# Optimization experiments

Measured on AMD Instinct MI355X. Metric: run time of the kernel, lower is better.

Reference implementation:

```python
import jax, jax.numpy as jnp
import numpy as np

N_ELEC = 1536
SPINS = (768, 768)
L = 20.0
HID = 16


def _block_masks(spins, n):
    # blkdiag_mask: same-spin pairs (block diagonal); offdiag_mask: opposite-spin pairs
    cum = np.cumsum([0, *spins])
    off = np.ones((n, n), dtype=bool)
    for i, j in zip(cum[:-1], cum[1:]):
        off[i:j, i:j] = False
    return jnp.asarray(~off), jnp.asarray(off)


def _eta_mlp(s, W1, b1, W2, b2, W3, b3):
    # per-pair scalar MLP: (n,n) -> (n,n)
    h = jnp.tanh(s[..., None] * W1[0] + b1)      # (n,n,HID)
    h = jnp.tanh(h @ W2 + b2)                    # (n,n,HID)
    return (h @ W3 + b3)[..., 0]                 # (n,n)


def setup_inputs() -> dict:
    key = jax.random.key(0)
    ks = jax.random.split(key, 8)
    inp = {
        "x": jax.random.uniform(ks[0], (N_ELEC, 3), jnp.float32) * L,
        "cell": L * jnp.eye(3, dtype=jnp.float32),
        "Wp1": jax.random.normal(ks[1], (1, HID), jnp.float32),
        "bp1": jnp.zeros((HID,), jnp.float32),
        "Wp2": jax.random.normal(ks[2], (HID, HID), jnp.float32) / np.sqrt(HID),
        "bp2": jnp.zeros((HID,), jnp.float32),
        "Wp3": jax.random.normal(ks[3], (HID, 1), jnp.float32) / np.sqrt(HID),
        "bp3": jnp.zeros((1,), jnp.float32),
        "Wa1": jax.random.normal(ks[4], (1, HID), jnp.float32),
        "ba1": jnp.zeros((HID,), jnp.float32),
        "Wa2": jax.random.normal(ks[5], (HID, HID), jnp.float32) / np.sqrt(HID),
        "ba2": jnp.zeros((HID,), jnp.float32),
        "Wa3": jax.random.normal(ks[6], (HID, 1), jnp.float32) / np.sqrt(HID),
        "ba3": jnp.zeros((1,), jnp.float32),
        "n_up": SPINS[0],
    }
    return inp


def reference(x, cell, Wp1, bp1, Wp2, bp2, Wp3, bp3,
              Wa1, ba1, Wa2, ba2, Wa3, ba3, n_up):
    n = x.shape[-2]
    ndim = 3
    spins = (int(n_up), n - int(n_up))
    blkdiag_mask, offdiag_mask = _block_masks(spins, n)

    # r_s of the homogeneous electron gas
    vol_pp = jnp.abs(jnp.linalg.det(cell)) / n
    rs = (2 * (ndim - 1) * jnp.pi / (ndim * vol_pp)) ** (-1.0 / ndim)

    # periodic (half-sinusoid) displacement features
    frac = x @ jnp.linalg.inv(cell)                      # (n,3)
    d_frac = frac[:, None, :] - frac[None, :, :]         # (n,n,3)
    d_hsin = jnp.sin(jnp.pi * d_frac) @ cell / jnp.pi    # (n,n,3)
    eye = jnp.eye(n, dtype=x.dtype)
    # safe norm: diagonal pairs are masked out of eta anyway
    dist = jnp.sqrt(jnp.sum(d_hsin * d_hsin, axis=-1) + eye)

    x_by_rs = dist / rs
    eta = _eta_mlp(x_by_rs, Wp1, bp1, Wp2, bp2, Wp3, bp3) * blkdiag_mask * (1 - eye)
    eta = eta + _eta_mlp(x_by_rs, Wa1, ba1, Wa2, ba2, Wa3, ba3) * offdiag_mask

    dr = jnp.einsum('ij,ijl->jl', eta, -d_hsin)          # (n,3)
    return x + dr
```

## Files before the change

### kernel.cpp

```cpp
#include <hip/hip_runtime.h>
#include <math.h>

#define HID   16
#define BLK   256
#define TBL_N 4096

__device__ __forceinline__ float fast_tanh(float x) {
    float ax = fabsf(x);
    float t  = __expf(-2.0f * ax);
    float r  = (1.0f - t) * __builtin_amdgcn_rcpf(1.0f + t);
    return copysignf(r, x);
}

__device__ __forceinline__ float eta_mlp(float s,
    const float* __restrict__ W1, const float* __restrict__ b1,
    const float* __restrict__ W2, const float* __restrict__ b2,
    const float* __restrict__ W3, const float* __restrict__ b3)
{
    float g[HID];
#pragma unroll
    for (int l = 0; l < HID; ++l) g[l] = fast_tanh(fmaf(s, W1[l], b1[l]));
    float t[HID];
#pragma unroll
    for (int l = 0; l < HID; ++l) t[l] = b2[l];
#pragma unroll
    for (int m = 0; m < HID; ++m) {
        float gm = g[m];
#pragma unroll
        for (int l = 0; l < HID; ++l) t[l] = fmaf(gm, W2[m * HID + l], t[l]);
    }
    float eta = b3[0];
#pragma unroll
    for (int l = 0; l < HID; ++l) eta = fmaf(fast_tanh(t[l]), W3[l], eta);
    return eta;
}

__device__ __forceinline__ void derive_consts(const float* __restrict__ cell,
                                              int n, float* inv_rs, float* smax_s)
{
    const float m00=cell[0],m01=cell[1],m02=cell[2];
    const float m10=cell[3],m11=cell[4],m12=cell[5];
    const float m20=cell[6],m21=cell[7],m22=cell[8];
    const float det = m00*(m11*m22-m12*m21)-m01*(m10*m22-m12*m20)+m02*(m10*m21-m11*m20);
    const float PI = 3.14159265358979323846f;
    const float vol_pp = fabsf(det) / (float)n;
    *inv_rs = cbrtf(4.0f * PI / (3.0f * vol_pp));
    const float r0 = sqrtf(m00*m00+m01*m01+m02*m02);
    const float r1 = sqrtf(m10*m10+m11*m11+m12*m12);
    const float r2 = sqrtf(m20*m20+m21*m21+m22*m22);
    *smax_s = (r0 + r1 + r2) * (1.0f / PI) * (*inv_rs) * 1.0005f;
}

extern "C" __global__ void build_tables(
    const float* __restrict__ x, const float* __restrict__ cell,
    const float* __restrict__ Wp1, const float* __restrict__ bp1,
    const float* __restrict__ Wp2, const float* __restrict__ bp2,
    const float* __restrict__ Wp3, const float* __restrict__ bp3,
    const float* __restrict__ Wa1, const float* __restrict__ ba1,
    const float* __restrict__ Wa2, const float* __restrict__ ba2,
    const float* __restrict__ Wa3, const float* __restrict__ ba3,
    float2* __restrict__ tbl, float4* __restrict__ frac, int n)
{
    const int t = blockIdx.x * blockDim.x + threadIdx.x;

    if (t < 2 * TBL_N) {
        const int bank = (t >= TBL_N) ? 1 : 0;
        const int idx  = bank ? (t - TBL_N) : t;

        float inv_rs, smax;
        derive_consts(cell, n, &inv_rs, &smax);
        const float ds = smax / (float)(TBL_N - 1);
        const float s  = idx * ds;

        float v0, v1;
        if (bank == 0) {
            v0 = eta_mlp(s,      Wp1, bp1, Wp2, bp2, Wp3, bp3);
            v1 = eta_mlp(s + ds, Wp1, bp1, Wp2, bp2, Wp3, bp3);
        } else {
            v0 = eta_mlp(s,      Wa1, ba1, Wa2, ba2, Wa3, ba3);
            v1 = eta_mlp(s + ds, Wa1, ba1, Wa2, ba2, Wa3, ba3);
        }
        tbl[t] = make_float2(v0, v1 - v0);
        return;
    }

    const int i = t - 2 * TBL_N;
    if (i < n) {
        const float m00=cell[0],m01=cell[1],m02=cell[2];
        const float m10=cell[3],m11=cell[4],m12=cell[5];
        const float m20=cell[6],m21=cell[7],m22=cell[8];
        const float det = m00*(m11*m22-m12*m21)-m01*(m10*m22-m12*m20)+m02*(m10*m21-m11*m20);
        const float id  = 1.0f / det;
        const float i00=(m11*m22-m12*m21)*id, i01=(m02*m21-m01*m22)*id, i02=(m01*m12-m02*m11)*id;
        const float i10=(m12*m20-m10*m22)*id, i11=(m00*m22-m02*m20)*id, i12=(m02*m10-m00*m12)*id;
        const float i20=(m10*m21-m11*m20)*id, i21=(m01*m20-m00*m21)*id, i22=(m00*m11-m01*m10)*id;
        float x0 = x[i*3+0], x1 = x[i*3+1], x2 = x[i*3+2];
        float4 f;
        f.x = x0*i00 + x1*i10 + x2*i20;
        f.y = x0*i01 + x1*i11 + x2*i21;
        f.z = x0*i02 + x1*i12 + x2*i22;
        f.w = 0.0f;
        frac[i] = f;
    }
}

extern "C" __global__ __launch_bounds__(BLK)
void pair_backflow_main(
    const float* __restrict__ x, const float* __restrict__ cell,
    const int* __restrict__ n_up_ptr,
    const float2* __restrict__ tbl, const float4* __restrict__ frac,
    float* __restrict__ out, int n)
{
    __shared__ float sred[BLK / 64][3];

    const int tid = threadIdx.x;
    const int j   = blockIdx.x;

    const float m00=cell[0],m01=cell[1],m02=cell[2];
    const float m10=cell[3],m11=cell[4],m12=cell[5];
    const float m20=cell[6],m21=cell[7],m22=cell[8];
    const float IPI = 0.31830988618379067154f;
    const float c00=m00*IPI, c01=m01*IPI, c02=m02*IPI;
    const float c10=m10*IPI, c11=m11*IPI, c12=m12*IPI;
    const float c20=m20*IPI, c21=m21*IPI, c22=m22*IPI;

    float inv_rs, smax;
    derive_consts(cell, n, &inv_rs, &smax);
    const float c_u  = inv_rs * (float)(TBL_N - 1) / smax;
    const float umax = (float)(TBL_N - 1);

    const int  n_up = *n_up_ptr;
    const bool j_up = (j < n_up);
    const float4 fj = frac[j];

    float acc0 = 0.0f, acc1 = 0.0f, acc2 = 0.0f;

    for (int i = tid; i < n; i += BLK) {
        float4 fi = frac[i];
        float s0 = __builtin_amdgcn_sinf(0.5f * (fi.x - fj.x));
        float s1 = __builtin_amdgcn_sinf(0.5f * (fi.y - fj.y));
        float s2 = __builtin_amdgcn_sinf(0.5f * (fi.z - fj.z));
        float h0 = fmaf(s0, c00, fmaf(s1, c10, s2 * c20));
        float h1 = fmaf(s0, c01, fmaf(s1, c11, s2 * c21));
        float h2 = fmaf(s0, c02, fmaf(s1, c12, s2 * c22));
        float dist = sqrtf(fmaf(h0, h0, fmaf(h1, h1, h2 * h2)));

        float u   = fminf(dist * c_u, umax);
        int   idx = (int)u;
        float fr  = u - (float)idx;

        const bool same = ((i < n_up) == j_up);
        float2 e = tbl[(same ? 0 : TBL_N) + idx];
        float eta = fmaf(fr, e.y, e.x);
        eta = (i == j) ? 0.0f : eta;

        acc0 = fmaf(-eta, h0, acc0);
        acc1 = fmaf(-eta, h1, acc1);
        acc2 = fmaf(-eta, h2, acc2);
    }

#pragma unroll
    for (int off = 32; off > 0; off >>= 1) {
        acc0 += __shfl_xor(acc0, off);
        acc1 += __shfl_xor(acc1, off);
        acc2 += __shfl_xor(acc2, off);
    }
    const int lane = tid & 63;
    const int wid  = tid >> 6;
    if (lane == 0) {
        sred[wid][0] = acc0; sred[wid][1] = acc1; sred[wid][2] = acc2;
    }
    __syncthreads();
    if (tid < 3) {
        float dr = 0.0f;
#pragma unroll
        for (int wv = 0; wv < BLK / 64; ++wv) dr += sred[wv][tid];
        out[j * 3 + tid] = x[j * 3 + tid] + dr;
    }
}

extern "C" void kernel_launch(void* const* d_in, const int* in_sizes, int n_in,
                              void* d_out, int out_size, void* d_ws, size_t ws_size,
                              hipStream_t stream) {
    const float* x    = (const float*)d_in[0];
    const float* cell = (const float*)d_in[1];
    const float* Wp1  = (const float*)d_in[2];
    const float* bp1  = (const float*)d_in[3];
    const float* Wp2  = (const float*)d_in[4];
    const float* bp2  = (const float*)d_in[5];
    const float* Wp3  = (const float*)d_in[6];
    const float* bp3  = (const float*)d_in[7];
    const float* Wa1  = (const float*)d_in[8];
    const float* ba1  = (const float*)d_in[9];
    const float* Wa2  = (const float*)d_in[10];
    const float* ba2  = (const float*)d_in[11];
    const float* Wa3  = (const float*)d_in[12];
    const float* ba3  = (const float*)d_in[13];
    const int*   nup  = (const int*)d_in[14];
    float* out = (float*)d_out;

    const int n = in_sizes[0] / 3;

    float2* tbl  = (float2*)d_ws;
    float4* frac = (float4*)((char*)d_ws + (size_t)(2 * TBL_N) * sizeof(float2));

    const int work = 2 * TBL_N + n;
    build_tables<<<dim3((work + BLK - 1) / BLK), dim3(BLK), 0, stream>>>(
        x, cell, Wp1, bp1, Wp2, bp2, Wp3, bp3,
        Wa1, ba1, Wa2, ba2, Wa3, ba3, tbl, frac, n);

    pair_backflow_main<<<dim3(n), dim3(BLK), 0, stream>>>(
        x, cell, nup, tbl, frac, out, n);
}
```

Measured before the change: 97.72 us.

## Fuse table build and pair pass into one cooperative kernel, two rows per block

Merges the table-building and pair-accumulation kernels into a single cooperative launch separated by a grid-wide sync. Precomputed cell constants go into a small header, and spin flags plus half-angle scaling are packed into frac. Each block processes two output rows so every frac load is reused. The table stores single values, halving MLP evaluations, but lookups need two loads, and the grid sync plus the cooperative occupancy constraint are added costs.

```diff
diff --git a/kernel.cpp b/kernel.cpp
--- a/kernel.cpp
+++ b/kernel.cpp
@@ -1,9 +1,12 @@
 #include <hip/hip_runtime.h>
+#include <hip/hip_cooperative_groups.h>
 #include <math.h>
 
 #define HID   16
 #define BLK   256
 #define TBL_N 4096
+
+namespace cg = cooperative_groups;
 
 __device__ __forceinline__ float fast_tanh(float x) {
     float ax = fabsf(x);
@@ -51,41 +54,36 @@
     *smax_s = (r0 + r1 + r2) * (1.0f / PI) * (*inv_rs) * 1.0005f;
 }
 
-extern "C" __global__ void build_tables(
-    const float* __restrict__ x, const float* __restrict__ cell,
+extern "C" __global__ __launch_bounds__(BLK, 4)
+void pair_backflow_fused(
+    const float* __restrict__ x,   const float* __restrict__ cell,
     const float* __restrict__ Wp1, const float* __restrict__ bp1,
     const float* __restrict__ Wp2, const float* __restrict__ bp2,
     const float* __restrict__ Wp3, const float* __restrict__ bp3,
     const float* __restrict__ Wa1, const float* __restrict__ ba1,
     const float* __restrict__ Wa2, const float* __restrict__ ba2,
     const float* __restrict__ Wa3, const float* __restrict__ ba3,
-    float2* __restrict__ tbl, float4* __restrict__ frac, int n)
+    const int* __restrict__ n_up_ptr,
+    float* __restrict__ tbl, float4* __restrict__ frac, float* __restrict__ hdr,
+    float* __restrict__ out, int n)
 {
-    const int t = blockIdx.x * blockDim.x + threadIdx.x;
-
-    if (t < 2 * TBL_N) {
-        const int bank = (t >= TBL_N) ? 1 : 0;
-        const int idx  = bank ? (t - TBL_N) : t;
-
+    cg::grid_group gg = cg::this_grid();
+    const int tid = threadIdx.x;
+    const int g   = blockIdx.x * BLK + tid;
+
+    if (g <= 2 * TBL_N + 1) {
         float inv_rs, smax;
         derive_consts(cell, n, &inv_rs, &smax);
-        const float ds = smax / (float)(TBL_N - 1);
-        const float s  = idx * ds;
-
-        float v0, v1;
-        if (bank == 0) {
-            v0 = eta_mlp(s,      Wp1, bp1, Wp2, bp2, Wp3, bp3);
-            v1 = eta_mlp(s + ds, Wp1, bp1, Wp2, bp2, Wp3, bp3);
-        } else {
-            v0 = eta_mlp(s,      Wa1, ba1, Wa2, ba2, Wa3, ba3);
-            v1 = eta_mlp(s + ds, Wa1, ba1, Wa2, ba2, Wa3, ba3);
-        }
-        tbl[t] = make_float2(v0, v1 - v0);
-        return;
-    }
-
-    const int i = t - 2 * TBL_N;
-    if (i < n) {
+        const float ds  = smax / (float)(TBL_N - 1);
+        const int bank  = (g >= TBL_N) ? 1 : 0;
+        const int gg2   = (g >= 2 * TBL_N) ? (g - TBL_N) : g;
+        const int idx   = gg2 - bank * TBL_N;
+        const float s   = idx * ds;
+        float v = bank ? eta_mlp(s, Wa1, ba1, Wa2, ba2, Wa3, ba3)
+                       : eta_mlp(s, Wp1, bp1, Wp2, bp2, Wp3, bp3);
+        tbl[g] = v;
+    } else if (g < 2 * TBL_N + 2 + n) {
+        const int i = g - (2 * TBL_N + 2);
         const float m00=cell[0],m01=cell[1],m02=cell[2];
         const float m10=cell[3],m11=cell[4],m12=cell[5];
         const float m20=cell[6],m21=cell[7],m22=cell[8];
@@ -94,88 +92,105 @@
         const float i00=(m11*m22-m12*m21)*id, i01=(m02*m21-m01*m22)*id, i02=(m01*m12-m02*m11)*id;
         const float i10=(m12*m20-m10*m22)*id, i11=(m00*m22-m02*m20)*id, i12=(m02*m10-m00*m12)*id;
         const float i20=(m10*m21-m11*m20)*id, i21=(m01*m20-m00*m21)*id, i22=(m00*m11-m01*m10)*id;
+        const int n_up = *n_up_ptr;
         float x0 = x[i*3+0], x1 = x[i*3+1], x2 = x[i*3+2];
         float4 f;
-        f.x = x0*i00 + x1*i10 + x2*i20;
-        f.y = x0*i01 + x1*i11 + x2*i21;
-        f.z = x0*i02 + x1*i12 + x2*i22;
-        f.w = 0.0f;
+        f.x = 0.5f * (x0*i00 + x1*i10 + x2*i20);
+        f.y = 0.5f * (x0*i01 + x1*i11 + x2*i21);
+        f.z = 0.5f * (x0*i02 + x1*i12 + x2*i22);
+        f.w = (i < n_up) ? 0.0f : 1.0f;
         frac[i] = f;
-    }
-}
-
-extern "C" __global__ __launch_bounds__(BLK)
-void pair_backflow_main(
-    const float* __restrict__ x, const float* __restrict__ cell,
-    const int* __restrict__ n_up_ptr,
-    const float2* __restrict__ tbl, const float4* __restrict__ frac,
-    float* __restrict__ out, int n)
-{
-    __shared__ float sred[BLK / 64][3];
-
-    const int tid = threadIdx.x;
-    const int j   = blockIdx.x;
-
-    const float m00=cell[0],m01=cell[1],m02=cell[2];
-    const float m10=cell[3],m11=cell[4],m12=cell[5];
-    const float m20=cell[6],m21=cell[7],m22=cell[8];
-    const float IPI = 0.31830988618379067154f;
-    const float c00=m00*IPI, c01=m01*IPI, c02=m02*IPI;
-    const float c10=m10*IPI, c11=m11*IPI, c12=m12*IPI;
-    const float c20=m20*IPI, c21=m21*IPI, c22=m22*IPI;
-
-    float inv_rs, smax;
-    derive_consts(cell, n, &inv_rs, &smax);
-    const float c_u  = inv_rs * (float)(TBL_N - 1) / smax;
+    } else if (g == 2 * TBL_N + 2 + n) {
+        float inv_rs, smax;
+        derive_consts(cell, n, &inv_rs, &smax);
+        const float IPI = 0.31830988618379067154f;
+        hdr[0] = inv_rs * (float)(TBL_N - 1) / smax;
+        hdr[1] = cell[0]*IPI; hdr[2] = cell[1]*IPI; hdr[3] = cell[2]*IPI;
+        hdr[4] = cell[3]*IPI; hdr[5] = cell[4]*IPI; hdr[6] = cell[5]*IPI;
+        hdr[7] = cell[6]*IPI; hdr[8] = cell[7]*IPI; hdr[9] = cell[8]*IPI;
+    }
+
+    gg.sync();
+
+    const float c_u  = hdr[0];
+    const float c00 = hdr[1], c01 = hdr[2], c02 = hdr[3];
+    const float c10 = hdr[4], c11 = hdr[5], c12 = hdr[6];
+    const float c20 = hdr[7], c21 = hdr[8], c22 = hdr[9];
     const float umax = (float)(TBL_N - 1);
 
-    const int  n_up = *n_up_ptr;
-    const bool j_up = (j < n_up);
-    const float4 fj = frac[j];
-
-    float acc0 = 0.0f, acc1 = 0.0f, acc2 = 0.0f;
+    const int j0 = blockIdx.x;
+    const int j1 = blockIdx.x + (int)gridDim.x;
+    const bool has1 = (j1 < n);
+    const float4 fj0 = frac[j0];
+    const float4 fj1 = has1 ? frac[j1] : fj0;
+
+    float a00 = 0.0f, a01 = 0.0f, a02 = 0.0f;
+    float a10 = 0.0f, a11 = 0.0f, a12 = 0.0f;
 
     for (int i = tid; i < n; i += BLK) {
-        float4 fi = frac[i];
-        float s0 = __builtin_amdgcn_sinf(0.5f * (fi.x - fj.x));
-        float s1 = __builtin_amdgcn_sinf(0.5f * (fi.y - fj.y));
-        float s2 = __builtin_amdgcn_sinf(0.5f * (fi.z - fj.z));
-        float h0 = fmaf(s0, c00, fmaf(s1, c10, s2 * c20));
-        float h1 = fmaf(s0, c01, fmaf(s1, c11, s2 * c21));
-        float h2 = fmaf(s0, c02, fmaf(s1, c12, s2 * c22));
-        float dist = sqrtf(fmaf(h0, h0, fmaf(h1, h1, h2 * h2)));
-
-        float u   = fminf(dist * c_u, umax);
-        int   idx = (int)u;
-        float fr  = u - (float)idx;
-
-        const bool same = ((i < n_up) == j_up);
-        float2 e = tbl[(same ? 0 : TBL_N) + idx];
-        float eta = fmaf(fr, e.y, e.x);
-        eta = (i == j) ? 0.0f : eta;
-
-        acc0 = fmaf(-eta, h0, acc0);
-        acc1 = fmaf(-eta, h1, acc1);
-        acc2 = fmaf(-eta, h2, acc2);
+        const float4 fi = frac[i];
+
+        {
+            float s0 = __builtin_amdgcn_sinf(fi.x - fj0.x);
+            float s1 = __builtin_amdgcn_sinf(fi.y - fj0.y);
+            float s2 = __builtin_amdgcn_sinf(fi.z - fj0.z);
+            float h0 = fmaf(s0, c00, fmaf(s1, c10, s2 * c20));
+            float h1 = fmaf(s0, c01, fmaf(s1, c11, s2 * c21));
+            float h2 = fmaf(s0, c02, fmaf(s1, c12, s2 * c22));
+            float dist = sqrtf(fmaf(h0, h0, fmaf(h1, h1, h2 * h2)));
+            float u   = fminf(dist * c_u, umax);
+            int   idx = (int)u;
+            float fr  = u - (float)idx;
+            int   off = (fi.w != fj0.w) ? TBL_N : 0;
+            float e0 = tbl[off + idx];
+            float e1 = tbl[off + idx + 1];
+            float eta = fmaf(fr, e1 - e0, e0);
+            a00 = fmaf(-eta, h0, a00);
+            a01 = fmaf(-eta, h1, a01);
+            a02 = fmaf(-eta, h2, a02);
+        }
+        {
+            float s0 = __builtin_amdgcn_sinf(fi.x - fj1.x);
+            float s1 = __builtin_amdgcn_sinf(fi.y - fj1.y);
+            float s2 = __builtin_amdgcn_sinf(fi.z - fj1.z);
+            float h0 = fmaf(s0, c00, fmaf(s1, c10, s2 * c20));
+            float h1 = fmaf(s0, c01, fmaf(s1, c11, s2 * c21));
+            float h2 = fmaf(s0, c02, fmaf(s1, c12, s2 * c22));
+            float dist = sqrtf(fmaf(h0, h0, fmaf(h1, h1, h2 * h2)));
+            float u   = fminf(dist * c_u, umax);
+            int   idx = (int)u;
+            float fr  = u - (float)idx;
+            int   off = (fi.w != fj1.w) ? TBL_N : 0;
+            float e0 = tbl[off + idx];
+            float e1 = tbl[off + idx + 1];
+            float eta = fmaf(fr, e1 - e0, e0);
+            a10 = fmaf(-eta, h0, a10);
+            a11 = fmaf(-eta, h1, a11);
+            a12 = fmaf(-eta, h2, a12);
+        }
     }
 
 #pragma unroll
     for (int off = 32; off > 0; off >>= 1) {
-        acc0 += __shfl_xor(acc0, off);
-        acc1 += __shfl_xor(acc1, off);
-        acc2 += __shfl_xor(acc2, off);
-    }
+        a00 += __shfl_xor(a00, off); a01 += __shfl_xor(a01, off); a02 += __shfl_xor(a02, off);
+        a10 += __shfl_xor(a10, off); a11 += __shfl_xor(a11, off); a12 += __shfl_xor(a12, off);
+    }
+    __shared__ float sred[BLK / 64][6];
     const int lane = tid & 63;
     const int wid  = tid >> 6;
     if (lane == 0) {
-        sred[wid][0] = acc0; sred[wid][1] = acc1; sred[wid][2] = acc2;
+        sred[wid][0] = a00; sred[wid][1] = a01; sred[wid][2] = a02;
+        sred[wid][3] = a10; sred[wid][4] = a11; sred[wid][5] = a12;
     }
     __syncthreads();
-    if (tid < 3) {
+    if (tid < 6) {
         float dr = 0.0f;
 #pragma unroll
         for (int wv = 0; wv < BLK / 64; ++wv) dr += sred[wv][tid];
-        out[j * 3 + tid] = x[j * 3 + tid] + dr;
+        const int row  = (tid < 3) ? j0 : j1;
+        const int comp = (tid < 3) ? tid : (tid - 3);
+        if (tid < 3 || has1)
+            out[row * 3 + comp] = x[row * 3 + comp] + dr;
     }
 }
 
@@ -199,16 +214,20 @@
     const int*   nup  = (const int*)d_in[14];
     float* out = (float*)d_out;
 
-    const int n = in_sizes[0] / 3;
-
-    float2* tbl  = (float2*)d_ws;
-    float4* frac = (float4*)((char*)d_ws + (size_t)(2 * TBL_N) * sizeof(float2));
-
-    const int work = 2 * TBL_N + n;
-    build_tables<<<dim3((work + BLK - 1) / BLK), dim3(BLK), 0, stream>>>(
-        x, cell, Wp1, bp1, Wp2, bp2, Wp3, bp3,
-        Wa1, ba1, Wa2, ba2, Wa3, ba3, tbl, frac, n);
-
-    pair_backflow_main<<<dim3(n), dim3(BLK), 0, stream>>>(
-        x, cell, nup, tbl, frac, out, n);
-}
+    int n = in_sizes[0] / 3;
+
+    float*  tbl  = (float*)d_ws;
+    float4* frac = (float4*)((char*)d_ws + (64 << 10));
+    float*  hdr  = (float*)((char*)d_ws + (128 << 10));
+
+    int gridB = (n + 1) / 2;
+
+    void* args[] = {
+        (void*)&x, (void*)&cell,
+        (void*)&Wp1, (void*)&bp1, (void*)&Wp2, (void*)&bp2, (void*)&Wp3, (void*)&bp3,
+        (void*)&Wa1, (void*)&ba1, (void*)&Wa2, (void*)&ba2, (void*)&Wa3, (void*)&ba3,
+        (void*)&nup, (void*)&tbl, (void*)&frac, (void*)&hdr, (void*)&out, (void*)&n
+    };
+    hipLaunchCooperativeKernel((const void*)pair_backflow_fused,
+                               dim3(gridB), dim3(BLK), args, 0, stream);
+}
```

Result: slower. 162.9 us (+66.7%).
